# Performance work log

Measured on AMD Instinct MI355X. Metric: run time of the kernel, lower is better.

## Reference

```python
import jax, jax.numpy as jnp
import numpy as np

B, T, H, A = 64, 512, 1024, 256  # T == max_sen_len by construction of attention_u
PAD_VAL = -2.0 ** 22


def setup_inputs() -> dict:
    key = jax.random.key(0)
    k1, k2, k3, k4 = jax.random.split(key, 4)
    inputs = jax.random.normal(k1, (B, T, H), dtype=jnp.float32)
    sen_len = jax.random.randint(k2, (B,), 1, T + 1, dtype=jnp.int32)
    W = jax.random.normal(k3, (H, A), dtype=jnp.float32) * (1.0 / np.sqrt(H))
    b = jnp.zeros((A,), dtype=jnp.float32)
    U = jax.random.normal(k4, (A, T), dtype=jnp.float32) * (1.0 / np.sqrt(A))
    return {"inputs": inputs, "sen_len": sen_len, "W": W, "b": b, "U": U}


def reference(inputs, sen_len, W, b, U):
    # Dense with tanh: [B,T,H] @ [H,A] -> [B,T,A]
    alpha = jnp.tanh(jnp.einsum('bth,ha->bta', inputs, W) + b)
    # Score against attention_u: [B,T,A] @ [A,T] -> [B,T,T]
    scores = jnp.einsum('bta,as->bts', alpha, U)
    # sequence mask over last (key) dim, broadcast over query dim
    mask = jnp.arange(T)[None, :] < sen_len[:, None]        # [B,T]
    scores = jnp.where(mask[:, None, :], scores, jnp.float32(PAD_VAL))
    p = jax.nn.softmax(scores, axis=-1)                     # [B,T,T]
    # Weighted sum pooling: [B,T,T] @ [B,T,H] -> [B,T,H]
    Z = jnp.einsum('bts,bsh->bth', p, inputs)
    # dropout: is_training=False -> identity
    return Z
```

## Files before the change

### kernel.cpp

```cpp
#include <hip/hip_runtime.h>
#include <hip/hip_bf16.h>

typedef short short8 __attribute__((ext_vector_type(8)));
typedef short short4v __attribute__((ext_vector_type(4)));
typedef float f32x4 __attribute__((ext_vector_type(4)));
typedef __bf16 bf16x8 __attribute__((ext_vector_type(8)));

template <int ROWS>
__device__ __forceinline__ void stage2(const __hip_bfloat16* __restrict__ g,
                                       int ld, short* lds, int t) {
    const int w = t >> 6;
    const int lane = t & 63;
#pragma unroll
    for (int i = 0; i < ROWS / 64; ++i) {
        const int cb = i * 512 + w * 64;
        const int c = cb + lane;
        const int row = c >> 3;
        const int kc = (c & 7) ^ (row & 7);
        __builtin_amdgcn_global_load_lds((const void*)(g + (long)row * ld + kc * 8),
                                         (void*)(lds + cb * 8), 16, 0, 0);
    }
}

__global__ __launch_bounds__(512, 4) void gemm_xw_kernel(
    const float* __restrict__ Xf,
    const __hip_bfloat16* __restrict__ Wt,
    __hip_bfloat16* __restrict__ alpha,
    const float* __restrict__ bias) {
    __shared__ __align__(16) short smB[3][8192];
    __shared__ __align__(16) short smA[2][8192];

    int bx = blockIdx.x, by = blockIdx.y;
    {
        const int nx = gridDim.x, ny = gridDim.y;
        const int nwg = nx * ny;
        const int lin = bx + nx * by;
        const int swz = (lin & 7) * (nwg >> 3) + (lin >> 3);
        bx = swz % nx;
        by = swz / nx;
    }

    const int t = threadIdx.x;
    const int w = t >> 6, lane = t & 63;
    const int wm = w >> 1, wn = w & 1;
    const int fr = lane & 15, quad = lane >> 4;

    const float* Ab = Xf + (long)by * 128 * 1024;
    const __hip_bfloat16* Bb = Wt + (long)bx * 128 * 1024;

    int acs[2], arow[2], akc[2];
#pragma unroll
    for (int i = 0; i < 2; ++i) {
        acs[i] = i * 512 + t;
        arow[i] = acs[i] >> 3;
        akc[i] = ((acs[i] & 7) ^ (arow[i] & 7)) * 8;
    }

    f32x4 acc[2][4] = {};
    float4 rA[2][2];

#define XW_ISSUE_B(KT, BUF) stage2<128>(Bb + (KT) * 64, 1024, &smB[BUF][0], t);

#define XW_LOAD_A(KT)                                                           \
    _Pragma("unroll") for (int i = 0; i < 2; ++i) {                             \
        const float* src = Ab + (long)arow[i] * 1024 + (KT) * 64 + akc[i];      \
        rA[i][0] = *(const float4*)(src);                                       \
        rA[i][1] = *(const float4*)(src + 4);                                   \
    }

#define XW_WRITE_A(BUF)                                                         \
    _Pragma("unroll") for (int i = 0; i < 2; ++i) {                             \
        __hip_bfloat16 tmp[8] __attribute__((aligned(16)));                     \
        tmp[0] = __float2bfloat16(rA[i][0].x);                                  \
        tmp[1] = __float2bfloat16(rA[i][0].y);                                  \
        tmp[2] = __float2bfloat16(rA[i][0].z);                                  \
        tmp[3] = __float2bfloat16(rA[i][0].w);                                  \
        tmp[4] = __float2bfloat16(rA[i][1].x);                                  \
        tmp[5] = __float2bfloat16(rA[i][1].y);                                  \
        tmp[6] = __float2bfloat16(rA[i][1].z);                                  \
        tmp[7] = __float2bfloat16(rA[i][1].w);                                  \
        *(short8*)(void*)&smA[BUF][acs[i] * 8] = *(short8*)(void*)tmp;          \
    }

    XW_ISSUE_B(0, 0)
    XW_ISSUE_B(1, 1)
    XW_LOAD_A(0)
    XW_WRITE_A(0)
    XW_LOAD_A(1)
    __builtin_amdgcn_sched_barrier(0);
    asm volatile("s_waitcnt vmcnt(4)" ::: "memory");
    asm volatile("s_waitcnt lgkmcnt(0)" ::: "memory");
    __builtin_amdgcn_s_barrier();
    __builtin_amdgcn_sched_barrier(0);

#pragma unroll
    for (int k = 0; k < 16; ++k) {
        if (k + 2 < 16) XW_ISSUE_B(k + 2, (k + 2) % 3)
        {
            const short* At = &smA[k % 2][0];
            const short* Bt = &smB[k % 3][0];
#pragma unroll
            for (int ks = 0; ks < 2; ++ks) {
                bf16x8 af[2], bfv[4];
                const int kc = ks * 4 + quad;
#pragma unroll
                for (int m = 0; m < 2; ++m) {
                    const int row = wm * 32 + m * 16 + fr;
                    const int chunk = row * 8 + (kc ^ (row & 7));
                    af[m] = *(const bf16x8*)(const void*)(At + chunk * 8);
                }
#pragma unroll
                for (int n = 0; n < 4; ++n) {
                    const int row = wn * 64 + n * 16 + fr;
                    const int chunk = row * 8 + (kc ^ (row & 7));
                    bfv[n] = *(const bf16x8*)(const void*)(Bt + chunk * 8);
                }
#pragma unroll
                for (int m = 0; m < 2; ++m)
#pragma unroll
                    for (int n = 0; n < 4; ++n)
                        acc[m][n] = __builtin_amdgcn_mfma_f32_16x16x32_bf16(
                            af[m], bfv[n], acc[m][n], 0, 0, 0);
            }
        }
        if (k + 1 < 16) XW_WRITE_A((k + 1) % 2)
        if (k + 2 < 16) XW_LOAD_A(k + 2)
        __builtin_amdgcn_sched_barrier(0);
        if (k + 2 < 16) {
            asm volatile("s_waitcnt vmcnt(6)" ::: "memory");
        } else if (k + 1 < 16) {
            asm volatile("s_waitcnt vmcnt(0)" ::: "memory");
        }
        if (k + 1 < 16) {
            asm volatile("s_waitcnt lgkmcnt(0)" ::: "memory");
            __builtin_amdgcn_s_barrier();
            __builtin_amdgcn_sched_barrier(0);
        }
    }
#undef XW_ISSUE_B
#undef XW_LOAD_A
#undef XW_WRITE_A

    const long rowBase = (long)by * 128 + wm * 32;
    const int colBase = bx * 128 + wn * 64;
#pragma unroll
    for (int m = 0; m < 2; ++m) {
#pragma unroll
        for (int n = 0; n < 4; ++n) {
            const int col = colBase + n * 16 + fr;
            const float bv = bias[col];
#pragma unroll
            for (int j = 0; j < 4; ++j) {
                const long row = rowBase + m * 16 + quad * 4 + j;
                alpha[row * 256 + col] = __float2bfloat16(tanhf(acc[m][n][j] + bv));
            }
        }
    }
}

__global__ __launch_bounds__(512, 4) void gemm_pv_kernel(
    const __hip_bfloat16* __restrict__ P,
    const float* __restrict__ Xf,
    float* __restrict__ Z) {
    __shared__ __align__(16) short smA[3][8192];
    __shared__ __align__(16) short smB[2][5120];

    int bx = blockIdx.x, by = blockIdx.y, bz = blockIdx.z;
    {
        const int nx = gridDim.x, ny = gridDim.y;
        const int nwg = nx * ny * gridDim.z;
        const int lin = bx + nx * (by + ny * bz);
        const int swz = (lin & 7) * (nwg >> 3) + (lin >> 3);
        bx = swz % nx;
        const int r = swz / nx;
        by = r % ny;
        bz = r / ny;
    }

    const int t = threadIdx.x;
    const int w = t >> 6, lane = t & 63;
    const int wm = w >> 1, wn = w & 1;
    const int fr = lane & 15, quad = lane >> 4;

    const __hip_bfloat16* Ab = P + ((long)bz * 512 + by * 256) * 512;
    const float* Bb = Xf + (long)bz * 512 * 1024 + bx * 128;

    int acb[2], arow[2], akc[2];
#pragma unroll
    for (int i = 0; i < 2; ++i) {
        acb[i] = i * 512 + w * 64;
        const int s = acb[i] + lane;
        arow[i] = s >> 2;
        akc[i] = ((s & 3) ^ ((arow[i] >> 1) & 3)) * 8;
    }
    const int bi = t & 15;
    const int bhc = t >> 4;

    f32x4 acc[4][4] = {};
    float4 r0, r1;

#define PV_ISSUE_A(KT, BUF)                                                     \
    _Pragma("unroll") for (int i = 0; i < 2; ++i)                               \
        __builtin_amdgcn_global_load_lds(                                       \
            (const void*)(Ab + (long)arow[i] * 512 + (KT) * 32 + akc[i]),       \
            (void*)(&smA[BUF][acb[i] * 8]), 16, 0, 0);

#define PV_LOAD_B(KT)                                                           \
    {                                                                           \
        const float* s0 = Bb + (long)((KT) * 32 + 2 * bi) * 1024 + bhc * 4;     \
        r0 = *(const float4*)(s0);                                              \
        r1 = *(const float4*)(s0 + 1024);                                       \
    }

#define PV_WRITE_B(BUF)                                                         \
    {                                                                           \
        int* dst = (int*)(void*)&smB[BUF][(bhc * 4) * 40 + bi * 2];             \
        _Pragma("unroll") for (int j = 0; j < 4; ++j) {                         \
            __hip_bfloat16 h0 = __float2bfloat16(((const float*)&r0)[j]);       \
            __hip_bfloat16 h1 = __float2bfloat16(((const float*)&r1)[j]);       \
            dst[j * 20] = (int)*(unsigned short*)&h0 |                          \
                          ((int)*(unsigned short*)&h1 << 16);                   \
        }                                                                       \
    }

    PV_ISSUE_A(0, 0)
    PV_ISSUE_A(1, 1)
    PV_LOAD_B(0)
    PV_WRITE_B(0)
    PV_LOAD_B(1)
    __builtin_amdgcn_sched_barrier(0);
    asm volatile("s_waitcnt vmcnt(4)" ::: "memory");
    asm volatile("s_waitcnt lgkmcnt(0)" ::: "memory");
    __builtin_amdgcn_s_barrier();
    __builtin_amdgcn_sched_barrier(0);

#pragma unroll
    for (int k = 0; k < 16; ++k) {
        if (k + 2 < 16) PV_ISSUE_A(k + 2, (k + 2) % 3)
        {
            const short* At = &smA[k % 3][0];
            const short* Bt = &smB[k % 2][0];
            bf16x8 bfv[4];
#pragma unroll
            for (int n = 0; n < 4; ++n) {
                const int h = wn * 64 + n * 16 + fr;
                bfv[n] = *(const bf16x8*)(const void*)(Bt + h * 40 + quad * 8);
            }
#pragma unroll
            for (int m = 0; m < 4; ++m) {
                const int row = wm * 64 + m * 16 + fr;
                const int slot = row * 4 + (quad ^ ((row >> 1) & 3));
                const bf16x8 af = *(const bf16x8*)(const void*)(At + slot * 8);
#pragma unroll
                for (int n = 0; n < 4; ++n)
                    acc[m][n] = __builtin_amdgcn_mfma_f32_16x16x32_bf16(
                        af, bfv[n], acc[m][n], 0, 0, 0);
            }
        }
        if (k + 1 < 16) PV_WRITE_B((k + 1) % 2)
        if (k + 2 < 16) PV_LOAD_B(k + 2)
        __builtin_amdgcn_sched_barrier(0);
        if (k + 2 < 16) {
            asm volatile("s_waitcnt vmcnt(4)" ::: "memory");
        } else if (k + 1 < 16) {
            asm volatile("s_waitcnt vmcnt(0)" ::: "memory");
        }
        if (k + 1 < 16) {
            asm volatile("s_waitcnt lgkmcnt(0)" ::: "memory");
            __builtin_amdgcn_s_barrier();
            __builtin_amdgcn_sched_barrier(0);
        }
    }
#undef PV_ISSUE_A
#undef PV_LOAD_B
#undef PV_WRITE_B

    const long rowBase = (long)bz * 512 + by * 256 + wm * 64;
    const int colBase = bx * 128 + wn * 64;
#pragma unroll
    for (int m = 0; m < 4; ++m) {
#pragma unroll
        for (int n = 0; n < 4; ++n) {
            const int col = colBase + n * 16 + fr;
#pragma unroll
            for (int j = 0; j < 4; ++j) {
                const long row = rowBase + m * 16 + quad * 4 + j;
                Z[row * 1024 + col] = acc[m][n][j];
            }
        }
    }
}

__global__ __launch_bounds__(256) void transpose_cvt_kernel(const float* __restrict__ in,
                                                            __hip_bfloat16* __restrict__ out,
                                                            int R, int C) {
    const int o = blockIdx.x * 256 + threadIdx.x;
    if (o >= R * C) return;
    const int c = o / R;
    const int r = o - c * R;
    out[o] = __float2bfloat16(in[(long)r * C + c]);
}

__global__ __launch_bounds__(512) void score_softmax_kernel(
    const __hip_bfloat16* __restrict__ Aa,
    const __hip_bfloat16* __restrict__ Ut,
    __hip_bfloat16* __restrict__ P,
    const int* __restrict__ sen) {
    __shared__ __align__(16) short At[64 * 64];
    __shared__ __align__(16) short Bts[512 * 64];
    __shared__ float red[2][64][9];

    const int t = threadIdx.x;
    const int w = t >> 6, lane = t & 63;
    const int fr = lane & 15, quad = lane >> 4;
    const long row0 = (long)blockIdx.x * 64;
    const __hip_bfloat16* Ab = Aa + row0 * 256;

    f32x4 acc[4][4] = {};

    for (int kt = 0; kt < 4; ++kt) {
        if (kt) __syncthreads();
        {
            const int cb = w * 64;
            const int c = cb + lane;
            const int row = c >> 3, kc = (c & 7) ^ (row & 7);
            __builtin_amdgcn_global_load_lds(
                (const void*)(Ab + (long)row * 256 + kt * 64 + kc * 8),
                (void*)(At + cb * 8), 16, 0, 0);
        }
#pragma unroll
        for (int i = 0; i < 8; ++i) {
            const int cb = i * 512 + w * 64;
            const int c = cb + lane;
            const int row = c >> 3, kc = (c & 7) ^ (row & 7);
            __builtin_amdgcn_global_load_lds(
                (const void*)(Ut + (long)row * 256 + kt * 64 + kc * 8),
                (void*)(Bts + cb * 8), 16, 0, 0);
        }
        __syncthreads();
#pragma unroll
        for (int ks = 0; ks < 2; ++ks) {
            bf16x8 af[4], bfv[4];
            const int kc = ks * 4 + quad;
#pragma unroll
            for (int m = 0; m < 4; ++m) {
                const int row = m * 16 + fr;
                const int chunk = row * 8 + (kc ^ (row & 7));
                af[m] = *(const bf16x8*)(const void*)(At + chunk * 8);
            }
#pragma unroll
            for (int n = 0; n < 4; ++n) {
                const int row = w * 64 + n * 16 + fr;
                const int chunk = row * 8 + (kc ^ (row & 7));
                bfv[n] = *(const bf16x8*)(const void*)(Bts + chunk * 8);
            }
#pragma unroll
            for (int m = 0; m < 4; ++m)
#pragma unroll
                for (int n = 0; n < 4; ++n)
                    acc[m][n] = __builtin_amdgcn_mfma_f32_16x16x32_bf16(
                        af[m], bfv[n], acc[m][n], 0, 0, 0);
        }
    }
    __syncthreads();

    const int L = sen[row0 >> 9];
    bool valid[4];
#pragma unroll
    for (int n = 0; n < 4; ++n) valid[n] = (w * 64 + n * 16 + fr) < L;

    float mx[4][4];
#pragma unroll
    for (int m = 0; m < 4; ++m)
#pragma unroll
        for (int j = 0; j < 4; ++j) {
            float v = -3.0e38f;
#pragma unroll
            for (int n = 0; n < 4; ++n)
                if (valid[n]) v = fmaxf(v, acc[m][n][j]);
#pragma unroll
            for (int off = 8; off >= 1; off >>= 1) v = fmaxf(v, __shfl_xor(v, off, 64));
            mx[m][j] = v;
        }
    if (fr == 0) {
#pragma unroll
        for (int m = 0; m < 4; ++m)
#pragma unroll
            for (int j = 0; j < 4; ++j) red[0][m * 16 + quad * 4 + j][w] = mx[m][j];
    }
    __syncthreads();
    float rmax[4][4];
#pragma unroll
    for (int m = 0; m < 4; ++m)
#pragma unroll
        for (int j = 0; j < 4; ++j) {
            const int row = m * 16 + quad * 4 + j;
            float v = red[0][row][0];
#pragma unroll
            for (int ww = 1; ww < 8; ++ww) v = fmaxf(v, red[0][row][ww]);
            rmax[m][j] = v;
        }

    float sum[4][4];
#pragma unroll
    for (int m = 0; m < 4; ++m)
#pragma unroll
        for (int j = 0; j < 4; ++j) {
            float s = 0.f;
#pragma unroll
            for (int n = 0; n < 4; ++n) {
                float e = valid[n] ? __expf(acc[m][n][j] - rmax[m][j]) : 0.f;
                acc[m][n][j] = e;
                s += e;
            }
#pragma unroll
            for (int off = 8; off >= 1; off >>= 1) s += __shfl_xor(s, off, 64);
            sum[m][j] = s;
        }
    if (fr == 0) {
#pragma unroll
        for (int m = 0; m < 4; ++m)
#pragma unroll
            for (int j = 0; j < 4; ++j) red[1][m * 16 + quad * 4 + j][w] = sum[m][j];
    }
    __syncthreads();
#pragma unroll
    for (int m = 0; m < 4; ++m)
#pragma unroll
        for (int j = 0; j < 4; ++j) {
            const int row = m * 16 + quad * 4 + j;
            float s = 0.f;
#pragma unroll
            for (int ww = 0; ww < 8; ++ww) s += red[1][row][ww];
            const float inv = 1.f / s;
#pragma unroll
            for (int n = 0; n < 4; ++n)
                P[(row0 + row) * 512 + w * 64 + n * 16 + fr] =
                    __float2bfloat16(acc[m][n][j] * inv);
        }
}

extern "C" void kernel_launch(void* const* d_in, const int* in_sizes, int n_in,
                              void* d_out, int out_size, void* d_ws, size_t ws_size,
                              hipStream_t stream) {
    const float* X = (const float*)d_in[0];
    const int* sen = (const int*)d_in[1];
    const float* W = (const float*)d_in[2];
    const float* bias = (const float*)d_in[3];
    const float* U = (const float*)d_in[4];
    float* out = (float*)d_out;

    const int B = 64, T = 512, H = 1024, A = 256;
    const long M = (long)B * T;

    char* ws = (char*)d_ws;
    __hip_bfloat16* Pbf = (__hip_bfloat16*)ws;
    __hip_bfloat16* Wt = (__hip_bfloat16*)(ws + M * T * 2);
    __hip_bfloat16* Ut = (__hip_bfloat16*)((char*)Wt + (long)H * A * 2);

    __hip_bfloat16* alpha = (__hip_bfloat16*)((char*)d_out + M * H * 2);

    transpose_cvt_kernel<<<(H * A) / 256, 256, 0, stream>>>(W, Wt, H, A);
    transpose_cvt_kernel<<<(A * T) / 256, 256, 0, stream>>>(U, Ut, A, T);
    gemm_xw_kernel<<<dim3(2, 256), 512, 0, stream>>>(X, Wt, alpha, bias);
    score_softmax_kernel<<<(int)(M / 64), 512, 0, stream>>>(alpha, Ut, Pbf, sen);
    gemm_pv_kernel<<<dim3(H / 128, T / 256, B), 512, 0, stream>>>(Pbf, X, out);
}
```

Measured before the change: 139.4 us.

## Deepen register prefetch pipelines and stream U operand directly into registers

```diff
diff --git a/kernel.cpp b/kernel.cpp
--- a/kernel.cpp
+++ b/kernel.cpp
@@ -57,86 +57,88 @@
     }
 
     f32x4 acc[2][4] = {};
-    float4 rA[2][2];
+    float4 rAs[2][2][2];
 
 #define XW_ISSUE_B(KT, BUF) stage2<128>(Bb + (KT) * 64, 1024, &smB[BUF][0], t);
 
-#define XW_LOAD_A(KT)                                                           \
+#define XW_LOAD_A(KT, S)                                                        \
     _Pragma("unroll") for (int i = 0; i < 2; ++i) {                             \
         const float* src = Ab + (long)arow[i] * 1024 + (KT) * 64 + akc[i];      \
-        rA[i][0] = *(const float4*)(src);                                       \
-        rA[i][1] = *(const float4*)(src + 4);                                   \
-    }
-
-#define XW_WRITE_A(BUF)                                                         \
+        rAs[S][i][0] = *(const float4*)(src);                                   \
+        rAs[S][i][1] = *(const float4*)(src + 4);                               \
+    }
+
+#define XW_WRITE_A(BUF, S)                                                      \
     _Pragma("unroll") for (int i = 0; i < 2; ++i) {                             \
         __hip_bfloat16 tmp[8] __attribute__((aligned(16)));                     \
-        tmp[0] = __float2bfloat16(rA[i][0].x);                                  \
-        tmp[1] = __float2bfloat16(rA[i][0].y);                                  \
-        tmp[2] = __float2bfloat16(rA[i][0].z);                                  \
-        tmp[3] = __float2bfloat16(rA[i][0].w);                                  \
-        tmp[4] = __float2bfloat16(rA[i][1].x);                                  \
-        tmp[5] = __float2bfloat16(rA[i][1].y);                                  \
-        tmp[6] = __float2bfloat16(rA[i][1].z);                                  \
-        tmp[7] = __float2bfloat16(rA[i][1].w);                                  \
+        tmp[0] = __float2bfloat16(rAs[S][i][0].x);                              \
+        tmp[1] = __float2bfloat16(rAs[S][i][0].y);                              \
+        tmp[2] = __float2bfloat16(rAs[S][i][0].z);                              \
+        tmp[3] = __float2bfloat16(rAs[S][i][0].w);                              \
+        tmp[4] = __float2bfloat16(rAs[S][i][1].x);                              \
+        tmp[5] = __float2bfloat16(rAs[S][i][1].y);                              \
+        tmp[6] = __float2bfloat16(rAs[S][i][1].z);                              \
+        tmp[7] = __float2bfloat16(rAs[S][i][1].w);                              \
         *(short8*)(void*)&smA[BUF][acs[i] * 8] = *(short8*)(void*)tmp;          \
     }
 
+    XW_LOAD_A(0, 0)
     XW_ISSUE_B(0, 0)
     XW_ISSUE_B(1, 1)
-    XW_LOAD_A(0)
-    XW_WRITE_A(0)
-    XW_LOAD_A(1)
-    __builtin_amdgcn_sched_barrier(0);
-    asm volatile("s_waitcnt vmcnt(4)" ::: "memory");
+    XW_WRITE_A(0, 0)
+    XW_LOAD_A(1, 1)
+    XW_LOAD_A(2, 0)
+    __builtin_amdgcn_sched_barrier(0);
+    asm volatile("s_waitcnt vmcnt(10)" ::: "memory");
     asm volatile("s_waitcnt lgkmcnt(0)" ::: "memory");
     __builtin_amdgcn_s_barrier();
     __builtin_amdgcn_sched_barrier(0);
 
-#pragma unroll
-    for (int k = 0; k < 16; ++k) {
-        if (k + 2 < 16) XW_ISSUE_B(k + 2, (k + 2) % 3)
-        {
-            const short* At = &smA[k % 2][0];
-            const short* Bt = &smB[k % 3][0];
-#pragma unroll
-            for (int ks = 0; ks < 2; ++ks) {
-                bf16x8 af[2], bfv[4];
-                const int kc = ks * 4 + quad;
-#pragma unroll
-                for (int m = 0; m < 2; ++m) {
-                    const int row = wm * 32 + m * 16 + fr;
-                    const int chunk = row * 8 + (kc ^ (row & 7));
-                    af[m] = *(const bf16x8*)(const void*)(At + chunk * 8);
-                }
-#pragma unroll
-                for (int n = 0; n < 4; ++n) {
-                    const int row = wn * 64 + n * 16 + fr;
-                    const int chunk = row * 8 + (kc ^ (row & 7));
-                    bfv[n] = *(const bf16x8*)(const void*)(Bt + chunk * 8);
-                }
-#pragma unroll
-                for (int m = 0; m < 2; ++m)
-#pragma unroll
-                    for (int n = 0; n < 4; ++n)
-                        acc[m][n] = __builtin_amdgcn_mfma_f32_16x16x32_bf16(
-                            af[m], bfv[n], acc[m][n], 0, 0, 0);
-            }
-        }
-        if (k + 1 < 16) XW_WRITE_A((k + 1) % 2)
-        if (k + 2 < 16) XW_LOAD_A(k + 2)
-        __builtin_amdgcn_sched_barrier(0);
-        if (k + 2 < 16) {
-            asm volatile("s_waitcnt vmcnt(6)" ::: "memory");
-        } else if (k + 1 < 16) {
-            asm volatile("s_waitcnt vmcnt(0)" ::: "memory");
-        }
-        if (k + 1 < 16) {
-            asm volatile("s_waitcnt lgkmcnt(0)" ::: "memory");
-            __builtin_amdgcn_s_barrier();
-            __builtin_amdgcn_sched_barrier(0);
-        }
-    }
+#define XW_STEP(K)                                                              \
+    {                                                                           \
+        if ((K) + 2 < 16) { XW_ISSUE_B((K) + 2, ((K) + 2) % 3) }                \
+        const short* At_ = &smA[(K) % 2][0];                                    \
+        const short* Bt_ = &smB[(K) % 3][0];                                    \
+        _Pragma("unroll") for (int ks = 0; ks < 2; ++ks) {                      \
+            bf16x8 af[2], bfv[4];                                               \
+            const int kc = ks * 4 + quad;                                       \
+            _Pragma("unroll") for (int m = 0; m < 2; ++m) {                     \
+                const int row = wm * 32 + m * 16 + fr;                          \
+                const int chunk = row * 8 + (kc ^ (row & 7));                   \
+                af[m] = *(const bf16x8*)(const void*)(At_ + chunk * 8);         \
+            }                                                                   \
+            _Pragma("unroll") for (int n = 0; n < 4; ++n) {                     \
+                const int row = wn * 64 + n * 16 + fr;                          \
+                const int chunk = row * 8 + (kc ^ (row & 7));                   \
+                bfv[n] = *(const bf16x8*)(const void*)(Bt_ + chunk * 8);        \
+            }                                                                   \
+            _Pragma("unroll") for (int m = 0; m < 2; ++m)                       \
+                _Pragma("unroll") for (int n = 0; n < 4; ++n)                   \
+                    acc[m][n] = __builtin_amdgcn_mfma_f32_16x16x32_bf16(        \
+                        af[m], bfv[n], acc[m][n], 0, 0, 0);                     \
+        }                                                                       \
+        if ((K) + 1 < 16) { XW_WRITE_A(((K) + 1) % 2, ((K) + 1) & 1) }          \
+        if ((K) + 3 < 16) { XW_LOAD_A((K) + 3, ((K) + 1) & 1) }                 \
+        __builtin_amdgcn_sched_barrier(0);                                      \
+        if ((K) + 3 < 16) {                                                     \
+            asm volatile("s_waitcnt vmcnt(10)" ::: "memory");                   \
+        } else if ((K) + 2 < 16) {                                              \
+            asm volatile("s_waitcnt vmcnt(6)" ::: "memory");                    \
+        } else if ((K) + 1 < 16) {                                              \
+            asm volatile("s_waitcnt vmcnt(0)" ::: "memory");                    \
+        }                                                                       \
+        if ((K) + 1 < 16) {                                                     \
+            asm volatile("s_waitcnt lgkmcnt(0)" ::: "memory");                  \
+            __builtin_amdgcn_s_barrier();                                       \
+            __builtin_amdgcn_sched_barrier(0);                                  \
+        }                                                                       \
+    }
+
+    XW_STEP(0)  XW_STEP(1)  XW_STEP(2)  XW_STEP(3)
+    XW_STEP(4)  XW_STEP(5)  XW_STEP(6)  XW_STEP(7)
+    XW_STEP(8)  XW_STEP(9)  XW_STEP(10) XW_STEP(11)
+    XW_STEP(12) XW_STEP(13) XW_STEP(14) XW_STEP(15)
+#undef XW_STEP
 #undef XW_ISSUE_B
 #undef XW_LOAD_A
 #undef XW_WRITE_A
@@ -197,7 +199,7 @@
     const int bhc = t >> 4;
 
     f32x4 acc[4][4] = {};
-    float4 r0, r1;
+    float4 r0s[2], r1s[2];
 
 #define PV_ISSUE_A(KT, BUF)                                                     \
     _Pragma("unroll") for (int i = 0; i < 2; ++i)                               \
@@ -205,19 +207,19 @@
             (const void*)(Ab + (long)arow[i] * 512 + (KT) * 32 + akc[i]),       \
             (void*)(&smA[BUF][acb[i] * 8]), 16, 0, 0);
 
-#define PV_LOAD_B(KT)                                                           \
+#define PV_LOAD_B(KT, S)                                                        \
     {                                                                           \
         const float* s0 = Bb + (long)((KT) * 32 + 2 * bi) * 1024 + bhc * 4;     \
-        r0 = *(const float4*)(s0);                                              \
-        r1 = *(const float4*)(s0 + 1024);                                       \
-    }
-
-#define PV_WRITE_B(BUF)                                                         \
+        r0s[S] = *(const float4*)(s0);                                          \
+        r1s[S] = *(const float4*)(s0 + 1024);                                   \
+    }
+
+#define PV_WRITE_B(BUF, S)                                                      \
     {                                                                           \
         int* dst = (int*)(void*)&smB[BUF][(bhc * 4) * 40 + bi * 2];             \
         _Pragma("unroll") for (int j = 0; j < 4; ++j) {                         \
-            __hip_bfloat16 h0 = __float2bfloat16(((const float*)&r0)[j]);       \
-            __hip_bfloat16 h1 = __float2bfloat16(((const float*)&r1)[j]);       \
+            __hip_bfloat16 h0 = __float2bfloat16(((const float*)&r0s[S])[j]);   \
+            __hip_bfloat16 h1 = __float2bfloat16(((const float*)&r1s[S])[j]);   \
             dst[j * 20] = (int)*(unsigned short*)&h0 |                          \
                           ((int)*(unsigned short*)&h1 << 16);                   \
         }                                                                       \
@@ -225,52 +227,56 @@
 
     PV_ISSUE_A(0, 0)
     PV_ISSUE_A(1, 1)
-    PV_LOAD_B(0)
-    PV_WRITE_B(0)
-    PV_LOAD_B(1)
-    __builtin_amdgcn_sched_barrier(0);
-    asm volatile("s_waitcnt vmcnt(4)" ::: "memory");
+    PV_LOAD_B(0, 0)
+    PV_WRITE_B(0, 0)
+    PV_LOAD_B(1, 1)
+    PV_LOAD_B(2, 0)
+    __builtin_amdgcn_sched_barrier(0);
+    asm volatile("s_waitcnt vmcnt(6)" ::: "memory");
     asm volatile("s_waitcnt lgkmcnt(0)" ::: "memory");
     __builtin_amdgcn_s_barrier();
     __builtin_amdgcn_sched_barrier(0);
 
-#pragma unroll
-    for (int k = 0; k < 16; ++k) {
-        if (k + 2 < 16) PV_ISSUE_A(k + 2, (k + 2) % 3)
-        {
-            const short* At = &smA[k % 3][0];
-            const short* Bt = &smB[k % 2][0];
-            bf16x8 bfv[4];
-#pragma unroll
-            for (int n = 0; n < 4; ++n) {
-                const int h = wn * 64 + n * 16 + fr;
-                bfv[n] = *(const bf16x8*)(const void*)(Bt + h * 40 + quad * 8);
-            }
-#pragma unroll
-            for (int m = 0; m < 4; ++m) {
-                const int row = wm * 64 + m * 16 + fr;
-                const int slot = row * 4 + (quad ^ ((row >> 1) & 3));
-                const bf16x8 af = *(const bf16x8*)(const void*)(At + slot * 8);
-#pragma unroll
-                for (int n = 0; n < 4; ++n)
-                    acc[m][n] = __builtin_amdgcn_mfma_f32_16x16x32_bf16(
-                        af, bfv[n], acc[m][n], 0, 0, 0);
-            }
-        }
-        if (k + 1 < 16) PV_WRITE_B((k + 1) % 2)
-        if (k + 2 < 16) PV_LOAD_B(k + 2)
-        __builtin_amdgcn_sched_barrier(0);
-        if (k + 2 < 16) {
-            asm volatile("s_waitcnt vmcnt(4)" ::: "memory");
-        } else if (k + 1 < 16) {
-            asm volatile("s_waitcnt vmcnt(0)" ::: "memory");
-        }
-        if (k + 1 < 16) {
-            asm volatile("s_waitcnt lgkmcnt(0)" ::: "memory");
-            __builtin_amdgcn_s_barrier();
-            __builtin_amdgcn_sched_barrier(0);
-        }
-    }
+#define PV_STEP(K)                                                              \
+    {                                                                           \
+        if ((K) + 2 < 16) { PV_ISSUE_A((K) + 2, ((K) + 2) % 3) }                \
+        const short* At_ = &smA[(K) % 3][0];                                    \
+        const short* Bt_ = &smB[(K) % 2][0];                                    \
+        bf16x8 bfv[4];                                                          \
+        _Pragma("unroll") for (int n = 0; n < 4; ++n) {                         \
+            const int h = wn * 64 + n * 16 + fr;                                \
+            bfv[n] = *(const bf16x8*)(const void*)(Bt_ + h * 40 + quad * 8);    \
+        }                                                                       \
+        _Pragma("unroll") for (int m = 0; m < 4; ++m) {                         \
+            const int row = wm * 64 + m * 16 + fr;                              \
+            const int slot = row * 4 + (quad ^ ((row >> 1) & 3));               \
+            const bf16x8 af = *(const bf16x8*)(const void*)(At_ + slot * 8);    \
+            _Pragma("unroll") for (int n = 0; n < 4; ++n)                       \
+                acc[m][n] = __builtin_amdgcn_mfma_f32_16x16x32_bf16(            \
+                    af, bfv[n], acc[m][n], 0, 0, 0);                            \
+        }                                                                       \
+        if ((K) + 1 < 16) { PV_WRITE_B(((K) + 1) % 2, ((K) + 1) & 1) }          \
+        if ((K) + 3 < 16) { PV_LOAD_B((K) + 3, ((K) + 1) & 1) }                 \
+        __builtin_amdgcn_sched_barrier(0);                                      \
+        if ((K) + 3 < 16) {                                                     \
+            asm volatile("s_waitcnt vmcnt(6)" ::: "memory");                    \
+        } else if ((K) + 2 < 16) {                                              \
+            asm volatile("s_waitcnt vmcnt(4)" ::: "memory");                    \
+        } else if ((K) + 1 < 16) {                                              \
+            asm volatile("s_waitcnt vmcnt(0)" ::: "memory");                    \
+        }                                                                       \
+        if ((K) + 1 < 16) {                                                     \
+            asm volatile("s_waitcnt lgkmcnt(0)" ::: "memory");                  \
+            __builtin_amdgcn_s_barrier();                                       \
+            __builtin_amdgcn_sched_barrier(0);                                  \
+        }                                                                       \
+    }
+
+    PV_STEP(0)  PV_STEP(1)  PV_STEP(2)  PV_STEP(3)
+    PV_STEP(4)  PV_STEP(5)  PV_STEP(6)  PV_STEP(7)
+    PV_STEP(8)  PV_STEP(9)  PV_STEP(10) PV_STEP(11)
+    PV_STEP(12) PV_STEP(13) PV_STEP(14) PV_STEP(15)
+#undef PV_STEP
 #undef PV_ISSUE_A
 #undef PV_LOAD_B
 #undef PV_WRITE_B
@@ -301,13 +307,12 @@
     out[o] = __float2bfloat16(in[(long)r * C + c]);
 }
 
-__global__ __launch_bounds__(512) void score_softmax_kernel(
+__global__ __launch_bounds__(512, 4) void score_softmax_kernel(
     const __hip_bfloat16* __restrict__ Aa,
     const __hip_bfloat16* __restrict__ Ut,
     __hip_bfloat16* __restrict__ P,
     const int* __restrict__ sen) {
-    __shared__ __align__(16) short At[64 * 64];
-    __shared__ __align__(16) short Bts[512 * 64];
+    __shared__ __align__(16) short At[2048 * 8];
     __shared__ float red[2][64][9];
 
     const int t = threadIdx.x;
@@ -316,52 +321,51 @@
     const long row0 = (long)blockIdx.x * 64;
     const __hip_bfloat16* Ab = Aa + row0 * 256;
 
+#pragma unroll
+    for (int i = 0; i < 4; ++i) {
+        const int cb = i * 512 + w * 64;
+        const int c = cb + lane;
+        const int row = c >> 5;
+        const int kc = (c & 31) ^ (row & 7);
+        __builtin_amdgcn_global_load_lds(
+            (const void*)(Ab + (long)row * 256 + kc * 8),
+            (void*)(At + cb * 8), 16, 0, 0);
+    }
+
     f32x4 acc[4][4] = {};
-
-    for (int kt = 0; kt < 4; ++kt) {
-        if (kt) __syncthreads();
-        {
-            const int cb = w * 64;
-            const int c = cb + lane;
-            const int row = c >> 3, kc = (c & 7) ^ (row & 7);
-            __builtin_amdgcn_global_load_lds(
-                (const void*)(Ab + (long)row * 256 + kt * 64 + kc * 8),
-                (void*)(At + cb * 8), 16, 0, 0);
-        }
-#pragma unroll
-        for (int i = 0; i < 8; ++i) {
-            const int cb = i * 512 + w * 64;
-            const int c = cb + lane;
-            const int row = c >> 3, kc = (c & 7) ^ (row & 7);
-            __builtin_amdgcn_global_load_lds(
-                (const void*)(Ut + (long)row * 256 + kt * 64 + kc * 8),
-                (void*)(Bts + cb * 8), 16, 0, 0);
-        }
-        __syncthreads();
-#pragma unroll
-        for (int ks = 0; ks < 2; ++ks) {
-            bf16x8 af[4], bfv[4];
-            const int kc = ks * 4 + quad;
-#pragma unroll
-            for (int m = 0; m < 4; ++m) {
-                const int row = m * 16 + fr;
-                const int chunk = row * 8 + (kc ^ (row & 7));
-                af[m] = *(const bf16x8*)(const void*)(At + chunk * 8);
-            }
-#pragma unroll
-            for (int n = 0; n < 4; ++n) {
-                const int row = w * 64 + n * 16 + fr;
-                const int chunk = row * 8 + (kc ^ (row & 7));
-                bfv[n] = *(const bf16x8*)(const void*)(Bts + chunk * 8);
-            }
-#pragma unroll
-            for (int m = 0; m < 4; ++m)
-#pragma unroll
-                for (int n = 0; n < 4; ++n)
-                    acc[m][n] = __builtin_amdgcn_mfma_f32_16x16x32_bf16(
-                        af[m], bfv[n], acc[m][n], 0, 0, 0);
-        }
-    }
+    bf16x8 bfvs[2][4];
+
+#define SM_LOAD_B(KT, S)                                                        \
+    _Pragma("unroll") for (int n = 0; n < 4; ++n)                               \
+        bfvs[S][n] = *(const bf16x8*)(const void*)(                             \
+            Ut + (w * 64 + n * 16 + fr) * 256 + (KT) * 32 + quad * 8);
+
+    SM_LOAD_B(0, 0)
+    SM_LOAD_B(1, 1)
+    __builtin_amdgcn_sched_barrier(0);
+    asm volatile("s_waitcnt vmcnt(8)" ::: "memory");
+    __builtin_amdgcn_s_barrier();
+    __builtin_amdgcn_sched_barrier(0);
+
+#define SM_STEP(KT)                                                             \
+    {                                                                           \
+        bf16x8 af[4];                                                           \
+        _Pragma("unroll") for (int m = 0; m < 4; ++m) {                         \
+            const int row = m * 16 + fr;                                        \
+            const int g = row * 32 + (((KT) * 4 + quad) ^ (row & 7));           \
+            af[m] = *(const bf16x8*)(const void*)(At + g * 8);                  \
+        }                                                                       \
+        _Pragma("unroll") for (int m = 0; m < 4; ++m)                           \
+            _Pragma("unroll") for (int n = 0; n < 4; ++n)                       \
+                acc[m][n] = __builtin_amdgcn_mfma_f32_16x16x32_bf16(            \
+                    af[m], bfvs[(KT) & 1][n], acc[m][n], 0, 0, 0);              \
+        if ((KT) + 2 < 8) { SM_LOAD_B((KT) + 2, (KT) & 1) }                     \
+    }
+
+    SM_STEP(0) SM_STEP(1) SM_STEP(2) SM_STEP(3)
+    SM_STEP(4) SM_STEP(5) SM_STEP(6) SM_STEP(7)
+#undef SM_STEP
+#undef SM_LOAD_B
     __syncthreads();
 
     const int L = sen[row0 >> 9];
```

Result: no change. 141.7 us (+1.6%).

## Load score B operand directly to registers and remap XCD block swizzles

Applied to the files above, without the earlier changes.

```diff
diff --git a/kernel.cpp b/kernel.cpp
--- a/kernel.cpp
+++ b/kernel.cpp
@@ -30,14 +30,13 @@
     __shared__ __align__(16) short smB[3][8192];
     __shared__ __align__(16) short smA[2][8192];
 
-    int bx = blockIdx.x, by = blockIdx.y;
+    int bx, by;
     {
-        const int nx = gridDim.x, ny = gridDim.y;
-        const int nwg = nx * ny;
-        const int lin = bx + nx * by;
-        const int swz = (lin & 7) * (nwg >> 3) + (lin >> 3);
-        bx = swz % nx;
-        by = swz / nx;
+        const int lin = blockIdx.x + 2 * blockIdx.y;
+        const int xcd = lin & 7;
+        const int idx = lin >> 3;
+        by = xcd * 32 + (idx >> 1);
+        bx = idx & 1;
     }
 
     const int t = threadIdx.x;
@@ -165,16 +164,15 @@
     __shared__ __align__(16) short smA[3][8192];
     __shared__ __align__(16) short smB[2][5120];
 
-    int bx = blockIdx.x, by = blockIdx.y, bz = blockIdx.z;
+    int bx, by, bz;
     {
-        const int nx = gridDim.x, ny = gridDim.y;
-        const int nwg = nx * ny * gridDim.z;
-        const int lin = bx + nx * (by + ny * bz);
-        const int swz = (lin & 7) * (nwg >> 3) + (lin >> 3);
-        bx = swz % nx;
-        const int r = swz / nx;
-        by = r % ny;
-        bz = r / ny;
+        const int lin = blockIdx.x + 8 * (blockIdx.y + 2 * blockIdx.z);
+        const int xcd = lin & 7;
+        const int idx = lin >> 3;
+        const int grp = xcd * 16 + (idx >> 3);
+        bx = idx & 7;
+        by = grp & 1;
+        bz = grp >> 1;
     }
 
     const int t = threadIdx.x;
@@ -301,13 +299,12 @@
     out[o] = __float2bfloat16(in[(long)r * C + c]);
 }
 
-__global__ __launch_bounds__(512) void score_softmax_kernel(
+__global__ __launch_bounds__(512, 4) void score_softmax_kernel(
     const __hip_bfloat16* __restrict__ Aa,
     const __hip_bfloat16* __restrict__ Ut,
     __hip_bfloat16* __restrict__ P,
     const int* __restrict__ sen) {
-    __shared__ __align__(16) short At[64 * 64];
-    __shared__ __align__(16) short Bts[512 * 64];
+    __shared__ __align__(16) short At[2048 * 8];
     __shared__ float red[2][64][9];
 
     const int t = threadIdx.x;
@@ -316,52 +313,51 @@
     const long row0 = (long)blockIdx.x * 64;
     const __hip_bfloat16* Ab = Aa + row0 * 256;
 
+#pragma unroll
+    for (int i = 0; i < 4; ++i) {
+        const int cb = i * 512 + w * 64;
+        const int c = cb + lane;
+        const int row = c >> 5;
+        const int kc = (c & 31) ^ (row & 7);
+        __builtin_amdgcn_global_load_lds(
+            (const void*)(Ab + (long)row * 256 + kc * 8),
+            (void*)(At + cb * 8), 16, 0, 0);
+    }
+
     f32x4 acc[4][4] = {};
-
-    for (int kt = 0; kt < 4; ++kt) {
-        if (kt) __syncthreads();
-        {
-            const int cb = w * 64;
-            const int c = cb + lane;
-            const int row = c >> 3, kc = (c & 7) ^ (row & 7);
-            __builtin_amdgcn_global_load_lds(
-                (const void*)(Ab + (long)row * 256 + kt * 64 + kc * 8),
-                (void*)(At + cb * 8), 16, 0, 0);
-        }
-#pragma unroll
-        for (int i = 0; i < 8; ++i) {
-            const int cb = i * 512 + w * 64;
-            const int c = cb + lane;
-            const int row = c >> 3, kc = (c & 7) ^ (row & 7);
-            __builtin_amdgcn_global_load_lds(
-                (const void*)(Ut + (long)row * 256 + kt * 64 + kc * 8),
-                (void*)(Bts + cb * 8), 16, 0, 0);
-        }
-        __syncthreads();
-#pragma unroll
-        for (int ks = 0; ks < 2; ++ks) {
-            bf16x8 af[4], bfv[4];
-            const int kc = ks * 4 + quad;
-#pragma unroll
-            for (int m = 0; m < 4; ++m) {
-                const int row = m * 16 + fr;
-                const int chunk = row * 8 + (kc ^ (row & 7));
-                af[m] = *(const bf16x8*)(const void*)(At + chunk * 8);
-            }
-#pragma unroll
-            for (int n = 0; n < 4; ++n) {
-                const int row = w * 64 + n * 16 + fr;
-                const int chunk = row * 8 + (kc ^ (row & 7));
-                bfv[n] = *(const bf16x8*)(const void*)(Bts + chunk * 8);
-            }
-#pragma unroll
-            for (int m = 0; m < 4; ++m)
-#pragma unroll
-                for (int n = 0; n < 4; ++n)
-                    acc[m][n] = __builtin_amdgcn_mfma_f32_16x16x32_bf16(
-                        af[m], bfv[n], acc[m][n], 0, 0, 0);
-        }
-    }
+    bf16x8 bfvs[2][4];
+
+#define SM_LOAD_B(KT, S)                                                        \
+    _Pragma("unroll") for (int n = 0; n < 4; ++n)                               \
+        bfvs[S][n] = *(const bf16x8*)(const void*)(                             \
+            Ut + (w * 64 + n * 16 + fr) * 256 + (KT) * 32 + quad * 8);
+
+    SM_LOAD_B(0, 0)
+    SM_LOAD_B(1, 1)
+    __builtin_amdgcn_sched_barrier(0);
+    asm volatile("s_waitcnt vmcnt(8)" ::: "memory");
+    __builtin_amdgcn_s_barrier();
+    __builtin_amdgcn_sched_barrier(0);
+
+#define SM_STEP(KT)                                                             \
+    {                                                                           \
+        bf16x8 af[4];                                                           \
+        _Pragma("unroll") for (int m = 0; m < 4; ++m) {                         \
+            const int row = m * 16 + fr;                                        \
+            const int g = row * 32 + (((KT) * 4 + quad) ^ (row & 7));           \
+            af[m] = *(const bf16x8*)(const void*)(At + g * 8);                  \
+        }                                                                       \
+        _Pragma("unroll") for (int m = 0; m < 4; ++m)                           \
+            _Pragma("unroll") for (int n = 0; n < 4; ++n)                       \
+                acc[m][n] = __builtin_amdgcn_mfma_f32_16x16x32_bf16(            \
+                    af[m], bfvs[(KT) & 1][n], acc[m][n], 0, 0, 0);              \
+        if ((KT) + 2 < 8) { SM_LOAD_B((KT) + 2, (KT) & 1) }                     \
+    }
+
+    SM_STEP(0) SM_STEP(1) SM_STEP(2) SM_STEP(3)
+    SM_STEP(4) SM_STEP(5) SM_STEP(6) SM_STEP(7)
+#undef SM_STEP
+#undef SM_LOAD_B
     __syncthreads();
 
     const int L = sen[row0 >> 9];
```

Measured after the change: 136.7 us. 2.0% less time.
